# Optimization experiments

Measured on AMD Instinct MI355X. Metric: run time of the kernel, lower is better.

## Reference

```python
import jax, jax.numpy as jnp
import numpy as np

B, S, D, H = 2, 2048, 1024, 16
HD = D // H
NEG = -10000000000.0

def setup_inputs() -> dict:
    key = jax.random.key(0)
    ks = jax.random.split(key, 9)
    s = 1.0 / np.sqrt(D)
    return {
        "x": jax.random.normal(ks[0], (B, S, D), dtype=jnp.float32),
        "Wq": jax.random.uniform(ks[1], (D, D), jnp.float32, -s, s),
        "bq": jax.random.uniform(ks[2], (D,), jnp.float32, -s, s),
        "Wk": jax.random.uniform(ks[3], (D, D), jnp.float32, -s, s),
        "bk": jax.random.uniform(ks[4], (D,), jnp.float32, -s, s),
        "Wv": jax.random.uniform(ks[5], (D, D), jnp.float32, -s, s),
        "bv": jax.random.uniform(ks[6], (D,), jnp.float32, -s, s),
        "Wo": jax.random.uniform(ks[7], (D, D), jnp.float32, -s, s),
        "bo": jax.random.uniform(ks[8], (D,), jnp.float32, -s, s),
    }

def reference(x, Wq, bq, Wk, bk, Wv, bv, Wo, bo):
    b, s, _ = x.shape
    def split_heads(t):
        return t.reshape(b, s, H, HD).transpose(0, 2, 1, 3)  # [b,h,s,hd]
    Q = split_heads(x @ Wq + bq)
    K = split_heads(x @ Wk + bk)
    V = split_heads(x @ Wv + bv)
    scores = jnp.einsum('bhqd,bhkd->bhqk', Q, K) / jnp.sqrt(jnp.float32(HD))
    causal = jnp.tril(jnp.ones((s, s), dtype=bool))
    scores = jnp.where(causal[None, None], scores, NEG)
    attn = jax.nn.softmax(scores, axis=-1)
    ctx = jnp.einsum('bhqk,bhkd->bhqd', attn, V)
    ctx = ctx.transpose(0, 2, 1, 3).reshape(b, s, D)
    return ctx @ Wo + bo
```

## Files before the change

kernel.cpp:

```cpp
#include <hip/hip_runtime.h>
#include <hip/hip_bf16.h>

#define BB 2
#define SS 2048
#define DD 1024
#define HH 16
#define HD 64
#define MM (BB*SS)

typedef __attribute__((ext_vector_type(8))) short bf16x8;
typedef __attribute__((ext_vector_type(4))) float f32x4;

#define QSCALE 0.18033688f

static __device__ __forceinline__ unsigned short f2bf(float f) {
    unsigned int u = __builtin_bit_cast(unsigned int, f);
    u += 0x7fffu + ((u >> 16) & 1u);
    return (unsigned short)(u >> 16);
}

static __device__ __forceinline__ void gload16(const unsigned short* g, unsigned short* l) {
    __builtin_amdgcn_global_load_lds(
        (const __attribute__((address_space(1))) unsigned int*)g,
        (__attribute__((address_space(3))) unsigned int*)l, 16, 0, 0);
}

__global__ __launch_bounds__(256) void prep_kernel(const float* __restrict__ x,
                                                   const float* __restrict__ W0,
                                                   const float* __restrict__ W1,
                                                   const float* __restrict__ W2,
                                                   const float* __restrict__ W3,
                                                   unsigned short* __restrict__ xb,
                                                   unsigned short* __restrict__ Wt)
{
    const int t = threadIdx.x;
    const int bid = blockIdx.x;
    if (bid < 2048) {
        const size_t i = ((size_t)bid * 256 + t) * 8;
        float4 a = *(const float4*)(x + i);
        float4 b = *(const float4*)(x + i + 4);
        union { unsigned short u[8]; bf16x8 v; } pk;
        pk.u[0] = f2bf(a.x); pk.u[1] = f2bf(a.y); pk.u[2] = f2bf(a.z); pk.u[3] = f2bf(a.w);
        pk.u[4] = f2bf(b.x); pk.u[5] = f2bf(b.y); pk.u[6] = f2bf(b.z); pk.u[7] = f2bf(b.w);
        *(bf16x8*)(xb + i) = pk.v;
        return;
    }
    __shared__ unsigned short Ts[64][72];
    const int wsel = (bid - 2048) >> 8;
    const int rem  = (bid - 2048) & 255;
    const float* W = wsel == 0 ? W0 : wsel == 1 ? W1 : wsel == 2 ? W2 : W3;
    unsigned short* out = Wt + (size_t)wsel * DD * DD;
    const int n0 = (rem & 15) * 64, k0 = (rem >> 4) * 64;
#pragma unroll
    for (int i = 0; i < 4; ++i) {
        const int r = (t >> 4) + i * 16;
        const int c = (t & 15) * 4;
        float4 v = *(const float4*)(W + (size_t)(k0 + r) * DD + n0 + c);
        Ts[c + 0][r] = f2bf(v.x); Ts[c + 1][r] = f2bf(v.y);
        Ts[c + 2][r] = f2bf(v.z); Ts[c + 3][r] = f2bf(v.w);
    }
    __syncthreads();
#pragma unroll
    for (int j = 0; j < 2; ++j) {
        const int ch = j * 256 + t;
        const int rn = ch >> 3, ck = (ch & 7) * 8;
        bf16x8 v = *(const bf16x8*)&Ts[rn][ck];
        *(bf16x8*)(out + (size_t)(n0 + rn) * DD + k0 + ck) = v;
    }
}

__global__ __launch_bounds__(256) void gemm_mfma(const unsigned short* __restrict__ A,
                                                 const unsigned short* __restrict__ Bt,
                                                 const float* __restrict__ bias0,
                                                 const float* __restrict__ bias1,
                                                 const float* __restrict__ bias2,
                                                 unsigned short* __restrict__ Qb,
                                                 unsigned short* __restrict__ Kb,
                                                 unsigned short* __restrict__ Vb,
                                                 float* __restrict__ outf,
                                                 int mode)
{
    __shared__ unsigned short As[128 * 64];
    __shared__ unsigned short Bs[128 * 64];

    const int t = threadIdx.x;
    const int w = t >> 6, l = t & 63;
    const int lane16 = l & 15, quad = l >> 4;
    const int m0 = blockIdx.x * 128, n0 = blockIdx.y * 128;
    const int wm = (w & 1) * 64, wn = (w >> 1) * 64;

    f32x4 acc[4][4] = {};

    int srow[4], skcg[4];
#pragma unroll
    for (int j = 0; j < 4; ++j) {
        const int c = t + j * 256;
        srow[j] = c >> 3;
        skcg[j] = (c & 7) ^ (srow[j] & 7);
    }

    for (int k0 = 0; k0 < DD; k0 += 64) {
        __syncthreads();
#pragma unroll
        for (int j = 0; j < 4; ++j) {
            const int c = t + j * 256;
            gload16(A  + (size_t)(m0 + srow[j]) * DD + k0 + skcg[j] * 8, As + c * 8);
            gload16(Bt + (size_t)(n0 + srow[j]) * DD + k0 + skcg[j] * 8, Bs + c * 8);
        }
        __syncthreads();

#pragma unroll
        for (int h = 0; h < 2; ++h) {
            bf16x8 af[4], bfr[4];
#pragma unroll
            for (int mt = 0; mt < 4; ++mt) {
                const int row = wm + mt * 16 + lane16;
                af[mt] = *(const bf16x8*)&As[(row * 8 + ((h * 4 + quad) ^ (row & 7))) * 8];
            }
#pragma unroll
            for (int nt = 0; nt < 4; ++nt) {
                const int row = wn + nt * 16 + lane16;
                bfr[nt] = *(const bf16x8*)&Bs[(row * 8 + ((h * 4 + quad) ^ (row & 7))) * 8];
            }
#pragma unroll
            for (int mt = 0; mt < 4; ++mt)
#pragma unroll
                for (int nt = 0; nt < 4; ++nt)
                    acc[mt][nt] = __builtin_amdgcn_mfma_f32_16x16x32_bf16(af[mt], bfr[nt], acc[mt][nt], 0, 0, 0);
        }
    }

    if (mode == 0) {
        const int which = n0 >> 10;
        const float* bias = which == 0 ? bias0 : which == 1 ? bias1 : bias2;
#pragma unroll
        for (int nt = 0; nt < 4; ++nt) {
            const int gcol = n0 + wn + nt * 16 + lane16;
            const int cd = gcol & 1023;
            const float bv = bias[cd];
            const int h_ = cd >> 6, d = cd & 63;
            if (which == 2) {
#pragma unroll
                for (int mt = 0; mt < 4; ++mt) {
                    const int row0 = m0 + wm + mt * 16 + quad * 4;
                    const int b_ = row0 >> 11, s0 = row0 & 2047;
                    union { unsigned short u[4]; uint2 v; } pk;
#pragma unroll
                    for (int r = 0; r < 4; ++r) pk.u[r] = f2bf(acc[mt][nt][r] + bv);
                    *(uint2*)(Vb + ((size_t)(b_ * HH + h_) * HD + d) * SS + s0) = pk.v;
                }
            } else {
                unsigned short* dst3 = which == 0 ? Qb : Kb;
                const float sc_ = which == 0 ? QSCALE : 1.0f;
#pragma unroll
                for (int mt = 0; mt < 4; ++mt)
#pragma unroll
                    for (int r = 0; r < 4; ++r) {
                        const int row = m0 + wm + mt * 16 + quad * 4 + r;
                        const int b_ = row >> 11, s_ = row & 2047;
                        dst3[(((size_t)(b_ * HH + h_) * SS + s_) * HD) + d] =
                            f2bf((acc[mt][nt][r] + bv) * sc_);
                    }
            }
        }
    } else {
#pragma unroll
        for (int nt = 0; nt < 4; ++nt) {
            const int gcol = n0 + wn + nt * 16 + lane16;
            const float bv = bias0[gcol];
#pragma unroll
            for (int mt = 0; mt < 4; ++mt)
#pragma unroll
                for (int r = 0; r < 4; ++r) {
                    const int row = m0 + wm + mt * 16 + quad * 4 + r;
                    outf[(size_t)row * DD + gcol] = acc[mt][nt][r] + bv;
                }
        }
    }
}

__global__ __launch_bounds__(512) void attn_mfma(const unsigned short* __restrict__ Q,
                                                 const unsigned short* __restrict__ K,
                                                 const unsigned short* __restrict__ V,
                                                 unsigned short* __restrict__ ctx)
{
    __shared__ unsigned short Ks[2][4096];
    __shared__ unsigned short Vs[2][4096];
    __shared__ unsigned short Ps[8][1280];

    const int t = threadIdx.x;
    const int w = t >> 6, l = t & 63;
    const int lane16 = l & 15, quad = l >> 4;
    const int bid = blockIdx.x;
    const int halfg = bid >> 8, idx = bid & 255;
    const int qb_ = idx >> 5;
    const int qblk = halfg ? qb_ : 15 - qb_;
    const int hb = idx & 31;
    const int h = hb & 15, b = hb >> 4;
    const int q0 = qblk * 128;
    const size_t bh = (size_t)(b * HH + h) * SS;
    const unsigned short* Vg = V + (size_t)(b * HH + h) * HD * SS;

    const int wrow0 = q0 + w * 16;
    bf16x8 qf0 = *(const bf16x8*)(Q + (bh + wrow0 + lane16) * HD + quad * 8);
    bf16x8 qf1 = *(const bf16x8*)(Q + (bh + wrow0 + lane16) * HD + 32 + quad * 8);

    f32x4 Oc[4] = {};
    float lpart[4] = {};

    const int ntiles = 2 * qblk + 2;
    const int sr = t >> 3;
    const int sg = (t & 7) ^ (sr & 7);

    {
        gload16(K  + (bh + sr) * HD + sg * 8, &Ks[0][t * 8]);
        gload16(Vg + (size_t)sr * SS + sg * 8, &Vs[0][t * 8]);
    }

    for (int kt = 0; kt < ntiles; ++kt) {
        __syncthreads();
        if (kt + 1 < ntiles) {
            const int k1 = (kt + 1) * 64;
            const int bi = (kt + 1) & 1;
            gload16(K  + (bh + k1 + sr) * HD + sg * 8, &Ks[bi][t * 8]);
            gload16(Vg + (size_t)sr * SS + k1 + sg * 8, &Vs[bi][t * 8]);
        }
        const int k0 = kt * 64;
        if (k0 > wrow0 + 15) continue;
        const unsigned short* Kt = Ks[kt & 1];
        const unsigned short* Vt = Vs[kt & 1];

        f32x4 sc[4] = {};
#pragma unroll
        for (int nt = 0; nt < 4; ++nt) {
            const int row = nt * 16 + lane16;
            bf16x8 k0f = *(const bf16x8*)&Kt[(row * 8 + (quad ^ (row & 7))) * 8];
            bf16x8 k1f = *(const bf16x8*)&Kt[(row * 8 + ((4 + quad) ^ (row & 7))) * 8];
            sc[nt] = __builtin_amdgcn_mfma_f32_16x16x32_bf16(qf0, k0f, sc[nt], 0, 0, 0);
            sc[nt] = __builtin_amdgcn_mfma_f32_16x16x32_bf16(qf1, k1f, sc[nt], 0, 0, 0);
        }

        float pr[4][4];
        if (k0 + 63 > wrow0) {
#pragma unroll
            for (int r = 0; r < 4; ++r) {
                const int row = wrow0 + quad * 4 + r;
#pragma unroll
                for (int nt = 0; nt < 4; ++nt)
                    if (k0 + nt * 16 + lane16 > row) sc[nt][r] = -1e30f;
            }
        }
#pragma unroll
        for (int nt = 0; nt < 4; ++nt)
#pragma unroll
            for (int r = 0; r < 4; ++r) pr[nt][r] = __builtin_amdgcn_exp2f(sc[nt][r]);
#pragma unroll
        for (int r = 0; r < 4; ++r)
            lpart[r] += (pr[0][r] + pr[1][r]) + (pr[2][r] + pr[3][r]);

        unsigned short* Pw = Ps[w];
#pragma unroll
        for (int nt = 0; nt < 4; ++nt) {
            const int plane = (nt >> 1) * 640, colin = (nt & 1) * 16 + lane16;
#pragma unroll
            for (int r = 0; r < 4; ++r)
                Pw[plane + (quad * 4 + r) * 40 + colin] = f2bf(pr[nt][r]);
        }
        bf16x8 pf0 = *(const bf16x8*)&Pw[lane16 * 40 + quad * 8];
        bf16x8 pf1 = *(const bf16x8*)&Pw[640 + lane16 * 40 + quad * 8];

#pragma unroll
        for (int dt = 0; dt < 4; ++dt) {
            const int drow = dt * 16 + lane16;
            bf16x8 v0 = *(const bf16x8*)&Vt[(drow * 8 + (quad ^ (drow & 7))) * 8];
            bf16x8 v1 = *(const bf16x8*)&Vt[(drow * 8 + ((4 + quad) ^ (drow & 7))) * 8];
            Oc[dt] = __builtin_amdgcn_mfma_f32_16x16x32_bf16(pf0, v0, Oc[dt], 0, 0, 0);
            Oc[dt] = __builtin_amdgcn_mfma_f32_16x16x32_bf16(pf1, v1, Oc[dt], 0, 0, 0);
        }
    }

#pragma unroll
    for (int off = 1; off < 16; off <<= 1)
#pragma unroll
        for (int r = 0; r < 4; ++r) lpart[r] += __shfl_xor(lpart[r], off);

#pragma unroll
    for (int r = 0; r < 4; ++r) {
        const float inv = 1.f / lpart[r];
        const int row = wrow0 + quad * 4 + r;
        unsigned short* dst = ctx + ((size_t)(b * SS) + row) * DD + h * HD + lane16;
#pragma unroll
        for (int dt = 0; dt < 4; ++dt) dst[dt * 16] = f2bf(Oc[dt][r] * inv);
    }
}

extern "C" void kernel_launch(void* const* d_in, const int* in_sizes, int n_in,
                              void* d_out, int out_size, void* d_ws, size_t ws_size,
                              hipStream_t stream) {
    const float* x  = (const float*)d_in[0];
    const float* Wq = (const float*)d_in[1];
    const float* bq = (const float*)d_in[2];
    const float* Wk = (const float*)d_in[3];
    const float* bk = (const float*)d_in[4];
    const float* Wv = (const float*)d_in[5];
    const float* bv = (const float*)d_in[6];
    const float* Wo = (const float*)d_in[7];
    const float* bo = (const float*)d_in[8];
    float* out = (float*)d_out;

    unsigned short* xb  = (unsigned short*)d_ws;
    unsigned short* Wt  = xb  + (size_t)MM * DD;
    unsigned short* Qb  = Wt  + (size_t)4 * DD * DD;
    unsigned short* Kb  = Qb  + (size_t)MM * DD;
    unsigned short* Vb  = Kb  + (size_t)MM * DD;
    unsigned short* ctxb = Vb + (size_t)MM * DD;

    prep_kernel<<<2048 + 1024, 256, 0, stream>>>(x, Wq, Wk, Wv, Wo, xb, Wt);

    gemm_mfma<<<dim3(MM / 128, 3072 / 128), 256, 0, stream>>>(
        xb, Wt, bq, bk, bv, Qb, Kb, Vb, nullptr, 0);

    attn_mfma<<<(SS / 128) * HH * BB, 512, 0, stream>>>(Qb, Kb, Vb, ctxb);

    gemm_mfma<<<dim3(MM / 128, DD / 128), 256, 0, stream>>>(
        ctxb, Wt + (size_t)3 * DD * DD, bo, nullptr, nullptr,
        nullptr, nullptr, nullptr, out, 1);
}
```

Measured before the change: 195.2 us.

## Stage QKV GEMM epilogue through LDS for vectorized stores and swizzle tile order

Remaps the workgroup index so that groups of 8 M-tiles are traversed together, which should improve L2 reuse of A and B tiles. The QKV projection epilogue now writes the bias-added bf16 results into shared memory with an XOR swizzle, then reads them back as 16-byte chunks and writes them to the head-split Q/K and transposed V layouts with coalesced vector stores. This replaces the scattered 2-byte and 8-byte global stores, at the cost of extra LDS traffic and barriers.

```diff
diff --git a/kernel.cpp b/kernel.cpp
--- a/kernel.cpp
+++ b/kernel.cpp
@@ -80,13 +80,23 @@
                                                  float* __restrict__ outf,
                                                  int mode)
 {
-    __shared__ unsigned short As[128 * 64];
-    __shared__ unsigned short Bs[128 * 64];
+    __shared__ unsigned short smem[2 * 128 * 64];
+    unsigned short* As = smem;
+    unsigned short* Bs = smem + 128 * 64;
 
     const int t = threadIdx.x;
     const int w = t >> 6, l = t & 63;
     const int lane16 = l & 15, quad = l >> 4;
-    const int m0 = blockIdx.x * 128, n0 = blockIdx.y * 128;
+
+    const int MT = gridDim.x, NTg = gridDim.y;
+    const int nwg = MT * NTg;
+    const int id = blockIdx.y * MT + blockIdx.x;
+    const int swz = (id & 7) * (nwg >> 3) + (id >> 3);
+    const int rg = swz % (8 * NTg);
+    const int mtile = (swz / (8 * NTg)) * 8 + (rg & 7);
+    const int ntile = rg >> 3;
+    const int m0 = mtile * 128, n0 = ntile * 128;
+
     const int wm = (w & 1) * 64, wn = (w >> 1) * 64;
 
     f32x4 acc[4][4] = {};
@@ -131,36 +141,63 @@
     }
 
     if (mode == 0) {
+        __syncthreads();
         const int which = n0 >> 10;
         const float* bias = which == 0 ? bias0 : which == 1 ? bias1 : bias2;
-#pragma unroll
-        for (int nt = 0; nt < 4; ++nt) {
-            const int gcol = n0 + wn + nt * 16 + lane16;
-            const int cd = gcol & 1023;
-            const float bv = bias[cd];
-            const int h_ = cd >> 6, d = cd & 63;
-            if (which == 2) {
+
+        if (which < 2) {
+            const float sc_ = which == 0 ? QSCALE : 1.0f;
+#pragma unroll
+            for (int nt = 0; nt < 4; ++nt) {
+                const int col = wn + nt * 16 + lane16;
+                const float bv = bias[(n0 + col) & 1023];
 #pragma unroll
                 for (int mt = 0; mt < 4; ++mt) {
-                    const int row0 = m0 + wm + mt * 16 + quad * 4;
-                    const int b_ = row0 >> 11, s0 = row0 & 2047;
-                    union { unsigned short u[4]; uint2 v; } pk;
-#pragma unroll
-                    for (int r = 0; r < 4; ++r) pk.u[r] = f2bf(acc[mt][nt][r] + bv);
-                    *(uint2*)(Vb + ((size_t)(b_ * HH + h_) * HD + d) * SS + s0) = pk.v;
+                    const int rb = wm + mt * 16 + quad * 4;
+                    const int sw = ((rb >> 2) & 3) << 5;
+#pragma unroll
+                    for (int r = 0; r < 4; ++r)
+                        smem[(rb + r) * 128 + (col ^ sw)] = f2bf((acc[mt][nt][r] + bv) * sc_);
                 }
-            } else {
-                unsigned short* dst3 = which == 0 ? Qb : Kb;
-                const float sc_ = which == 0 ? QSCALE : 1.0f;
-#pragma unroll
-                for (int mt = 0; mt < 4; ++mt)
-#pragma unroll
-                    for (int r = 0; r < 4; ++r) {
-                        const int row = m0 + wm + mt * 16 + quad * 4 + r;
-                        const int b_ = row >> 11, s_ = row & 2047;
-                        dst3[(((size_t)(b_ * HH + h_) * SS + s_) * HD) + d] =
-                            f2bf((acc[mt][nt][r] + bv) * sc_);
-                    }
+            }
+            __syncthreads();
+            unsigned short* dst0 = which == 0 ? Qb : Kb;
+#pragma unroll
+            for (int i = 0; i < 8; ++i) {
+                const int chunk = t + i * 256;
+                const int row = chunk >> 4, col8 = (chunk & 15) * 8;
+                bf16x8 v = *(const bf16x8*)&smem[row * 128 + (col8 ^ (((row >> 2) & 3) << 5))];
+                const int grow = m0 + row;
+                const int b_ = grow >> 11, s_ = grow & 2047;
+                const int cd = (n0 + col8) & 1023;
+                const int h_ = cd >> 6, d = cd & 63;
+                *(bf16x8*)(dst0 + ((size_t)(b_ * HH + h_) * SS + s_) * HD + d) = v;
+            }
+        } else {
+#pragma unroll
+            for (int nt = 0; nt < 4; ++nt) {
+                const int col = wn + nt * 16 + lane16;
+                const float bv = bias[(n0 + col) & 1023];
+                const int sw = (col & 7) << 3;
+#pragma unroll
+                for (int mt = 0; mt < 4; ++mt) {
+                    const int rb = wm + mt * 16 + quad * 4;
+#pragma unroll
+                    for (int r = 0; r < 4; ++r)
+                        smem[col * 128 + ((rb + r) ^ sw)] = f2bf(acc[mt][nt][r] + bv);
+                }
+            }
+            __syncthreads();
+            const int b_ = m0 >> 11;
+            const int sbase = m0 & 2047;
+#pragma unroll
+            for (int i = 0; i < 8; ++i) {
+                const int chunk = t + i * 256;
+                const int col = chunk >> 4, s8 = (chunk & 15) * 8;
+                bf16x8 v = *(const bf16x8*)&smem[col * 128 + (s8 ^ ((col & 7) << 3))];
+                const int cd = (n0 + col) & 1023;
+                const int h_ = cd >> 6, d = cd & 63;
+                *(bf16x8*)(Vb + ((size_t)(b_ * HH + h_) * HD + d) * SS + sbase + s8) = v;
             }
         }
     } else {
```

Result: no change. 197.2 us (+1.0%).
